# Performance work log

Measured on AMD Instinct MI355X. Metric: run time of the kernel, lower is better.

Reference implementation:

```python
import jax, jax.numpy as jnp
import numpy as np

LEAKY_SLOPE = 0.2  # alpha in the torch module
EPS = 1e-10

N_NODES = 100000
N_EDGES = 1600000
IN_F = 128
OUT_F = 64


def setup_inputs() -> dict:
    key = jax.random.key(0)
    k1, k2, k3, k4, k5 = jax.random.split(key, 5)
    h = jax.random.normal(k1, (N_NODES, IN_F), dtype=jnp.float32)
    W = jax.random.normal(k2, (IN_F, OUT_F), dtype=jnp.float32) * (1.0 / np.sqrt(IN_F))
    a1 = jax.random.normal(k3, (OUT_F,), dtype=jnp.float32) * 0.1
    a2 = jax.random.normal(k4, (OUT_F,), dtype=jnp.float32) * 0.1
    edge_index = jax.random.randint(k5, (2, N_EDGES), 0, N_NODES, dtype=jnp.int32)
    return {"h": h, "W": W, "a1": a1, "a2": a2, "edge_index": edge_index}


def reference(h, W, a1, a2, edge_index):
    # h: [N, in_f], W: [in_f, out_f], a1/a2: [out_f], edge_index: [2, E]
    N = h.shape[0]
    Wh = h @ W                                   # [N, out_f]
    row, col = edge_index[0], edge_index[1]      # [E]
    f1 = Wh @ a1                                 # [N]
    f2 = Wh @ a2                                 # [N]
    e = jax.nn.leaky_relu(f1[row] + f2[col], negative_slope=LEAKY_SLOPE)  # [E]
    e_exp = jnp.exp(e - jnp.max(e))              # global-max shift, as in torch code
    exp_sum = jax.ops.segment_sum(e_exp, row, num_segments=N)            # [N]
    alpha = e_exp / (exp_sum[row] + EPS)         # [E]  (dropout is identity in eval)
    weighted_Wh = Wh[col] * alpha[:, None]       # [E, out_f]
    h_prime = jax.ops.segment_sum(weighted_Wh, row, num_segments=N)      # [N, out_f]
    return jax.nn.elu(h_prime)                   # concat=True path
```

## Files before the change

### kernel.cpp

```cpp
#include <hip/hip_runtime.h>
#include <hip/hip_bf16.h>

#define N_NODES 100000
#define N_EDGES 1600000
#define IN_F 128
#define OUT_F 64

#define RPB 64
#define NB  1563
#define C_CHUNKS 250
#define CHUNK 6400
#define M_CNT (NB * C_CHUNKS)
#define SCANA_BLOCKS ((M_CNT + 1023) / 1024)

typedef __attribute__((ext_vector_type(8))) short short8;
typedef __attribute__((ext_vector_type(4))) float f32x4;

#define LDS_PITCH 136

__device__ __forceinline__ unsigned short f2bf(float x) {
    unsigned u = __float_as_uint(x);
    return (unsigned short)((u + 0x7FFFu + ((u >> 16) & 1u)) >> 16);
}
__device__ __forceinline__ float bf2f_u(unsigned short b) {
    return __uint_as_float((unsigned)b << 16);
}

__global__ __launch_bounds__(1024) void k_hist(
    const int* __restrict__ ei, int* __restrict__ cnt,
    const float* __restrict__ W, const float* __restrict__ a1,
    const float* __restrict__ a2, float* __restrict__ wa1, float* __restrict__ wa2)
{
    __shared__ int hl[NB];
    const int c = blockIdx.x;
    if (c == C_CHUNKS) {
        const int k = threadIdx.x;
        if (k < IN_F) {
            float s1 = 0.f, s2 = 0.f;
            #pragma unroll 8
            for (int f = 0; f < OUT_F; f++) {
                const float w = W[k * OUT_F + f];
                s1 += w * a1[f];
                s2 += w * a2[f];
            }
            wa1[k] = s1;
            wa2[k] = s2;
        }
        return;
    }
    for (int i = threadIdx.x; i < NB; i += 1024) hl[i] = 0;
    __syncthreads();
    const int e0 = c * CHUNK;
    for (int i = threadIdx.x; i < CHUNK; i += 1024)
        atomicAdd(&hl[ei[e0 + i] >> 6], 1);
    __syncthreads();
    for (int b = threadIdx.x; b < NB; b += 1024)
        cnt[b * C_CHUNKS + c] = hl[b];
}

__global__ __launch_bounds__(256) void k_gemm(
    const float* __restrict__ h, const float* __restrict__ W,
    const float* __restrict__ wa1, const float* __restrict__ wa2,
    unsigned short* __restrict__ Whb, float* __restrict__ f1, float* __restrict__ f2)
{
    __shared__ unsigned short Wt[OUT_F * LDS_PITCH];
    __shared__ unsigned short Al[16 * LDS_PITCH];

    const int tid  = threadIdx.x;
    const int lane = tid & 63;
    const int wav  = tid >> 6;
    const int quad = lane >> 4;
    const int nl   = lane & 15;

    for (int i = tid; i < IN_F * OUT_F; i += 256) {
        const int k = i >> 6, f = i & 63;
        Wt[f * LDS_PITCH + k] = f2bf(W[i]);
    }
    __syncthreads();

    short8 bfrag[4];
    #pragma unroll
    for (int ch = 0; ch < 4; ch++)
        bfrag[ch] = *(const short8*)&Wt[(wav * 16 + nl) * LDS_PITCH + ch * 32 + quad * 8];

    const int srow = tid >> 4;
    const int sc   = tid & 15;
    float w1r[8], w2r[8];
    #pragma unroll
    for (int j = 0; j < 8; j++) { w1r[j] = wa1[sc * 8 + j]; w2r[j] = wa2[sc * 8 + j]; }

    const int ntiles = N_NODES / 16;
    for (int tile = blockIdx.x; tile < ntiles; tile += gridDim.x) {
        const int base = tile * 16;
        __syncthreads();

        const float4 v0 = *(const float4*)&h[(base + srow) * IN_F + sc * 8];
        const float4 v1 = *(const float4*)&h[(base + srow) * IN_F + sc * 8 + 4];
        float p1 = v0.x * w1r[0] + v0.y * w1r[1] + v0.z * w1r[2] + v0.w * w1r[3]
                 + v1.x * w1r[4] + v1.y * w1r[5] + v1.z * w1r[6] + v1.w * w1r[7];
        float p2 = v0.x * w2r[0] + v0.y * w2r[1] + v0.z * w2r[2] + v0.w * w2r[3]
                 + v1.x * w2r[4] + v1.y * w2r[5] + v1.z * w2r[6] + v1.w * w2r[7];
        #pragma unroll
        for (int m = 8; m >= 1; m >>= 1) {
            p1 += __shfl_xor(p1, m, 64);
            p2 += __shfl_xor(p2, m, 64);
        }
        if (sc == 0) { f1[base + srow] = p1; f2[base + srow] = p2; }

        uint4 packed;
        packed.x = (unsigned)f2bf(v0.x) | ((unsigned)f2bf(v0.y) << 16);
        packed.y = (unsigned)f2bf(v0.z) | ((unsigned)f2bf(v0.w) << 16);
        packed.z = (unsigned)f2bf(v1.x) | ((unsigned)f2bf(v1.y) << 16);
        packed.w = (unsigned)f2bf(v1.z) | ((unsigned)f2bf(v1.w) << 16);
        *(uint4*)&Al[srow * LDS_PITCH + sc * 8] = packed;

        __syncthreads();

        f32x4 acc = {0.f, 0.f, 0.f, 0.f};
        #pragma unroll
        for (int ch = 0; ch < 4; ch++) {
            const short8 afrag = *(const short8*)&Al[nl * LDS_PITCH + ch * 32 + quad * 8];
            acc = __builtin_amdgcn_mfma_f32_16x16x32_bf16(afrag, bfrag[ch], acc, 0, 0, 0);
        }

        const int col = wav * 16 + nl;
        #pragma unroll
        for (int r = 0; r < 4; r++)
            Whb[(base + quad * 4 + r) * OUT_F + col] = f2bf(acc[r]);
    }
}

__global__ __launch_bounds__(256) void k_scanA(const int* __restrict__ cnt,
                                               int* __restrict__ bsum)
{
    __shared__ int sd[256];
    const int t = threadIdx.x;
    const int i0 = blockIdx.x * 1024 + t * 4;
    int s = 0;
    #pragma unroll
    for (int k = 0; k < 4; k++) {
        const int i = i0 + k;
        s += (i < M_CNT) ? cnt[i] : 0;
    }
    sd[t] = s; __syncthreads();
    for (int off = 128; off >= 1; off >>= 1) {
        if (t < off) sd[t] += sd[t + off];
        __syncthreads();
    }
    if (t == 0) bsum[blockIdx.x] = sd[0];
}

__global__ __launch_bounds__(256) void k_scanC(int* __restrict__ cnt,
                                               const int* __restrict__ bsum)
{
    __shared__ int red[256];
    __shared__ int ts[256];
    const int t = threadIdx.x;

    int pv = 0;
    for (int i = t; i < (int)blockIdx.x; i += 256) pv += bsum[i];
    red[t] = pv; __syncthreads();
    for (int off = 128; off >= 1; off >>= 1) {
        if (t < off) red[t] += red[t + off];
        __syncthreads();
    }
    const int bpref = red[0];

    const int i0 = blockIdx.x * 1024 + t * 4;
    int v[4]; int s = 0;
    #pragma unroll
    for (int k = 0; k < 4; k++) {
        const int i = i0 + k;
        v[k] = (i < M_CNT) ? cnt[i] : 0;
        s += v[k];
    }
    ts[t] = s; __syncthreads();
    for (int off = 1; off < 256; off <<= 1) {
        const int x = (t >= off) ? ts[t - off] : 0;
        __syncthreads();
        ts[t] += x;
        __syncthreads();
    }
    int excl = ts[t] - s + bpref;
    #pragma unroll
    for (int k = 0; k < 4; k++) {
        const int i = i0 + k;
        if (i < M_CNT) cnt[i] = excl;
        excl += v[k];
    }
}

__global__ __launch_bounds__(1024) void k_scatter(
    const int* __restrict__ ei,
    const float* __restrict__ f1,
    const float* __restrict__ f2,
    const int* __restrict__ cnt,
    uint2* __restrict__ pairs)
{
    __shared__ int cur[NB];
    const int c = blockIdx.x;
    for (int b = threadIdx.x; b < NB; b += 1024)
        cur[b] = cnt[b * C_CHUNKS + c];
    __syncthreads();

    const int e0 = c * CHUNK;
    for (int i = threadIdx.x; i < CHUNK; i += 1024) {
        const int r  = ei[e0 + i];
        const int cl = ei[N_EDGES + e0 + i];
        float x = f1[r] + f2[cl];
        x = (x >= 0.f) ? x : 0.2f * x;
        const float ee = __expf(x);
        const int pos = atomicAdd(&cur[r >> 6], 1);
        pairs[pos] = make_uint2(((unsigned)(r & 63) << 17) | (unsigned)cl,
                                __float_as_uint(ee));
    }
}

__global__ __launch_bounds__(256) void k_sort(
    const int* __restrict__ cnt,
    const uint2* __restrict__ pairs,
    uint2* __restrict__ pairs2,
    int* __restrict__ rowptr)
{
    __shared__ int cnt64[64];
    __shared__ int cur64[64];

    const int b   = blockIdx.x;
    const int tid = threadIdx.x;
    const int start = cnt[b * C_CHUNKS];
    const int end   = (b == NB - 1) ? N_EDGES : cnt[(b + 1) * C_CHUNKS];

    if (tid < 64) cnt64[tid] = 0;
    __syncthreads();

    for (int i = start + tid; i < end; i += 256)
        atomicAdd(&cnt64[pairs[i].x >> 17], 1);
    __syncthreads();

    if (tid < 64) {
        const int v = cnt64[tid];
        int s = v;
        #pragma unroll
        for (int off = 1; off < 64; off <<= 1) {
            const int x = __shfl_up(s, off, 64);
            if (tid >= off) s += x;
        }
        cur64[tid] = s - v;
        const int g = b * 64 + tid;
        if (g < N_NODES) rowptr[g] = start + s - v;
    }
    __syncthreads();

    for (int i = start + tid; i < end; i += 256) {
        const uint2 p = pairs[i];
        const int pos = atomicAdd(&cur64[p.x >> 17], 1);
        pairs2[start + pos] = p;
    }
    if (b == 0 && tid == 0) rowptr[N_NODES] = N_EDGES;
}

__global__ __launch_bounds__(256) void k_agg(
    const int* __restrict__ rowptr,
    const uint2* __restrict__ pairs2,
    const unsigned short* __restrict__ Whb,
    float* __restrict__ out)
{
    const int wid  = (blockIdx.x * 256 + threadIdx.x) >> 6;
    const int lane = threadIdx.x & 63;
    if (wid >= N_NODES) return;

    const int start = rowptr[wid];
    const int end   = rowptr[wid + 1];

    float acc = 0.f, s = 0.f;
    int j = start;

    for (; j + 8 <= end; j += 8) {
        uint2 p[8];
        #pragma unroll
        for (int k = 0; k < 8; k++) p[k] = pairs2[j + k];
        float wh[8];
        #pragma unroll
        for (int k = 0; k < 8; k++)
            wh[k] = bf2f_u(Whb[(((int)(p[k].x & 0x1FFFFu)) << 6) + lane]);
        #pragma unroll
        for (int k = 0; k < 8; k++) {
            const float ee = __uint_as_float(p[k].y);
            acc += ee * wh[k];
            s   += ee;
        }
    }
    for (; j + 4 <= end; j += 4) {
        uint2 p[4];
        #pragma unroll
        for (int k = 0; k < 4; k++) p[k] = pairs2[j + k];
        float wh[4];
        #pragma unroll
        for (int k = 0; k < 4; k++)
            wh[k] = bf2f_u(Whb[(((int)(p[k].x & 0x1FFFFu)) << 6) + lane]);
        #pragma unroll
        for (int k = 0; k < 4; k++) {
            const float ee = __uint_as_float(p[k].y);
            acc += ee * wh[k];
            s   += ee;
        }
    }
    for (; j < end; j++) {
        const uint2 p = pairs2[j];
        const float ee = __uint_as_float(p.y);
        acc += ee * bf2f_u(Whb[(((int)(p.x & 0x1FFFFu)) << 6) + lane]);
        s   += ee;
    }

    const float r = acc / (s + 1e-10f);
    out[wid * OUT_F + lane] = (r > 0.f) ? r : expm1f(r);
}

extern "C" void kernel_launch(void* const* d_in, const int* in_sizes, int n_in,
                              void* d_out, int out_size, void* d_ws, size_t ws_size,
                              hipStream_t stream) {
    const float* h  = (const float*)d_in[0];
    const float* W  = (const float*)d_in[1];
    const float* a1 = (const float*)d_in[2];
    const float* a2 = (const float*)d_in[3];
    const int* ei   = (const int*)d_in[4];
    float* out      = (float*)d_out;

    float* ws = (float*)d_ws;
    unsigned short* Whb = (unsigned short*)ws;
    float* f1     = ws + 3200000;
    float* f2     = f1 + N_NODES;
    float* wa1    = f2 + N_NODES;
    float* wa2    = wa1 + 128;
    int*   cnt    = (int*)(wa2 + 128);
    int*   bsum   = cnt + M_CNT;
    int*   rowptr = bsum + 384;
    int*   pad    = rowptr + 100002;
    if ((size_t)(pad - (int*)ws) & 1) pad++;
    uint2* pairs  = (uint2*)pad;
    uint2* pairs2 = pairs + N_EDGES;

    k_hist   <<<C_CHUNKS + 1, 1024, 0, stream>>>(ei, cnt, W, a1, a2, wa1, wa2);
    k_scanA  <<<SCANA_BLOCKS, 256, 0, stream>>>(cnt, bsum);
    k_scanC  <<<SCANA_BLOCKS, 256, 0, stream>>>(cnt, bsum);
    k_gemm   <<<1250, 256, 0, stream>>>(h, W, wa1, wa2, Whb, f1, f2);
    k_scatter<<<C_CHUNKS, 1024, 0, stream>>>(ei, f1, f2, cnt, pairs);
    k_sort   <<<NB, 256, 0, stream>>>(cnt, pairs, pairs2, rowptr);
    k_agg    <<<(N_NODES * 64 + 255) / 256, 256, 0, stream>>>(rowptr, pairs2, Whb, out);
}
```

Before: 228.3 us.

## Fuse per-bucket sort and aggregation into one block-level LDS-atomic kernel

Removes the second-level sort kernel and the per-row aggregation kernel. Each block now takes its 64-row bucket of unsorted pairs, splits it across four waves, and accumulates weighted Wh rows and exp sums into shared memory with atomics before applying normalization and ELU. This saves a full pass that reads and writes the pairs array, plus one launch. In exchange it adds LDS atomic contention and uses fewer, larger blocks.

Result: slower. 774.6 us (+239.3%).

```diff
diff --git a/kernel.cpp b/kernel.cpp
--- a/kernel.cpp
+++ b/kernel.cpp
@@ -216,69 +216,35 @@
     }
 }
 
-__global__ __launch_bounds__(256) void k_sort(
+__global__ __launch_bounds__(256) void k_aggb(
     const int* __restrict__ cnt,
     const uint2* __restrict__ pairs,
-    uint2* __restrict__ pairs2,
-    int* __restrict__ rowptr)
-{
-    __shared__ int cnt64[64];
-    __shared__ int cur64[64];
-
-    const int b   = blockIdx.x;
-    const int tid = threadIdx.x;
+    const unsigned short* __restrict__ Whb,
+    float* __restrict__ out)
+{
+    __shared__ float acc[64 * 64];
+    __shared__ float ssum[64];
+
+    const int b    = blockIdx.x;
+    const int tid  = threadIdx.x;
+    const int lane = tid & 63;
+    const int wav  = tid >> 6;
+
+    for (int i = tid; i < 64 * 64; i += 256) acc[i] = 0.f;
+    if (tid < 64) ssum[tid] = 0.f;
+    __syncthreads();
+
     const int start = cnt[b * C_CHUNKS];
     const int end   = (b == NB - 1) ? N_EDGES : cnt[(b + 1) * C_CHUNKS];
-
-    if (tid < 64) cnt64[tid] = 0;
-    __syncthreads();
-
-    for (int i = start + tid; i < end; i += 256)
-        atomicAdd(&cnt64[pairs[i].x >> 17], 1);
-    __syncthreads();
-
-    if (tid < 64) {
-        const int v = cnt64[tid];
-        int s = v;
-        #pragma unroll
-        for (int off = 1; off < 64; off <<= 1) {
-            const int x = __shfl_up(s, off, 64);
-            if (tid >= off) s += x;
-        }
-        cur64[tid] = s - v;
-        const int g = b * 64 + tid;
-        if (g < N_NODES) rowptr[g] = start + s - v;
-    }
-    __syncthreads();
-
-    for (int i = start + tid; i < end; i += 256) {
-        const uint2 p = pairs[i];
-        const int pos = atomicAdd(&cur64[p.x >> 17], 1);
-        pairs2[start + pos] = p;
-    }
-    if (b == 0 && tid == 0) rowptr[N_NODES] = N_EDGES;
-}
-
-__global__ __launch_bounds__(256) void k_agg(
-    const int* __restrict__ rowptr,
-    const uint2* __restrict__ pairs2,
-    const unsigned short* __restrict__ Whb,
-    float* __restrict__ out)
-{
-    const int wid  = (blockIdx.x * 256 + threadIdx.x) >> 6;
-    const int lane = threadIdx.x & 63;
-    if (wid >= N_NODES) return;
-
-    const int start = rowptr[wid];
-    const int end   = rowptr[wid + 1];
-
-    float acc = 0.f, s = 0.f;
-    int j = start;
-
-    for (; j + 8 <= end; j += 8) {
+    const int len   = end - start;
+    const int w0 = start + (len * wav) / 4;
+    const int w1 = start + (len * (wav + 1)) / 4;
+
+    int j = w0;
+    for (; j + 8 <= w1; j += 8) {
         uint2 p[8];
         #pragma unroll
-        for (int k = 0; k < 8; k++) p[k] = pairs2[j + k];
+        for (int k = 0; k < 8; k++) p[k] = pairs[j + k];
         float wh[8];
         #pragma unroll
         for (int k = 0; k < 8; k++)
@@ -286,14 +252,15 @@
         #pragma unroll
         for (int k = 0; k < 8; k++) {
             const float ee = __uint_as_float(p[k].y);
-            acc += ee * wh[k];
-            s   += ee;
-        }
-    }
-    for (; j + 4 <= end; j += 4) {
+            const int rl   = (int)(p[k].x >> 17);
+            atomicAdd(&acc[rl * 64 + lane], ee * wh[k]);
+            if (lane == 0) atomicAdd(&ssum[rl], ee);
+        }
+    }
+    for (; j + 4 <= w1; j += 4) {
         uint2 p[4];
         #pragma unroll
-        for (int k = 0; k < 4; k++) p[k] = pairs2[j + k];
+        for (int k = 0; k < 4; k++) p[k] = pairs[j + k];
         float wh[4];
         #pragma unroll
         for (int k = 0; k < 4; k++)
@@ -301,19 +268,28 @@
         #pragma unroll
         for (int k = 0; k < 4; k++) {
             const float ee = __uint_as_float(p[k].y);
-            acc += ee * wh[k];
-            s   += ee;
-        }
-    }
-    for (; j < end; j++) {
-        const uint2 p = pairs2[j];
+            const int rl   = (int)(p[k].x >> 17);
+            atomicAdd(&acc[rl * 64 + lane], ee * wh[k]);
+            if (lane == 0) atomicAdd(&ssum[rl], ee);
+        }
+    }
+    for (; j < w1; j++) {
+        const uint2 p = pairs[j];
         const float ee = __uint_as_float(p.y);
-        acc += ee * bf2f_u(Whb[(((int)(p.x & 0x1FFFFu)) << 6) + lane]);
-        s   += ee;
-    }
-
-    const float r = acc / (s + 1e-10f);
-    out[wid * OUT_F + lane] = (r > 0.f) ? r : expm1f(r);
+        const int rl   = (int)(p.x >> 17);
+        atomicAdd(&acc[rl * 64 + lane],
+                  ee * bf2f_u(Whb[(((int)(p.x & 0x1FFFFu)) << 6) + lane]));
+        if (lane == 0) atomicAdd(&ssum[rl], ee);
+    }
+    __syncthreads();
+
+    for (int rl = wav; rl < 64; rl += 4) {
+        const int g = b * 64 + rl;
+        if (g < N_NODES) {
+            const float r = acc[rl * 64 + lane] / (ssum[rl] + 1e-10f);
+            out[g * OUT_F + lane] = (r > 0.f) ? r : expm1f(r);
+        }
+    }
 }
 
 extern "C" void kernel_launch(void* const* d_in, const int* in_sizes, int n_in,
@@ -338,13 +314,11 @@
     int*   pad    = rowptr + 100002;
     if ((size_t)(pad - (int*)ws) & 1) pad++;
     uint2* pairs  = (uint2*)pad;
-    uint2* pairs2 = pairs + N_EDGES;
 
     k_hist   <<<C_CHUNKS + 1, 1024, 0, stream>>>(ei, cnt, W, a1, a2, wa1, wa2);
     k_scanA  <<<SCANA_BLOCKS, 256, 0, stream>>>(cnt, bsum);
     k_scanC  <<<SCANA_BLOCKS, 256, 0, stream>>>(cnt, bsum);
     k_gemm   <<<1250, 256, 0, stream>>>(h, W, wa1, wa2, Whb, f1, f2);
     k_scatter<<<C_CHUNKS, 1024, 0, stream>>>(ei, f1, f2, cnt, pairs);
-    k_sort   <<<NB, 256, 0, stream>>>(cnt, pairs, pairs2, rowptr);
-    k_agg    <<<(N_NODES * 64 + 255) / 256, 256, 0, stream>>>(rowptr, pairs2, Whb, out);
-}
+    k_aggb   <<<NB, 256, 0, stream>>>(cnt, pairs, Whb, out);
+}
```

## Fuse histogram with GEMM and bucket sort with aggregation kernels

Applied to the files above, without the earlier changes.

Merges the edge histogram and the node GEMM into one launch, with blocks split by role and LDS shared through a union. Each GEMM block now computes W·a1/W·a2 itself, so the separate reduction block goes away. Also fuses the per-bucket sort with aggregation: each block sorts its 64-row bucket, keeps the row pointers in LDS, then its 4 waves each aggregate 16 rows, with no global rowptr and no separate agg launch. This cuts the launch count from 7 to 5 and the rowptr round trip, but lowers aggregation parallelism to 4 waves per 64 rows and repeats the wa computation in every GEMM block.

After: 281.8 us. +23.4%, slower.

```diff
diff --git a/kernel.cpp b/kernel.cpp
--- a/kernel.cpp
+++ b/kernel.cpp
@@ -12,6 +12,7 @@
 #define CHUNK 6400
 #define M_CNT (NB * C_CHUNKS)
 #define SCANA_BLOCKS ((M_CNT + 1023) / 1024)
+#define GEMM_BLOCKS 1250
 
 typedef __attribute__((ext_vector_type(8))) short short8;
 typedef __attribute__((ext_vector_type(4))) float f32x4;
@@ -26,47 +27,35 @@
     return __uint_as_float((unsigned)b << 16);
 }
 
-__global__ __launch_bounds__(1024) void k_hist(
+__global__ __launch_bounds__(256) void k_histgemm(
     const int* __restrict__ ei, int* __restrict__ cnt,
-    const float* __restrict__ W, const float* __restrict__ a1,
-    const float* __restrict__ a2, float* __restrict__ wa1, float* __restrict__ wa2)
-{
-    __shared__ int hl[NB];
-    const int c = blockIdx.x;
-    if (c == C_CHUNKS) {
-        const int k = threadIdx.x;
-        if (k < IN_F) {
-            float s1 = 0.f, s2 = 0.f;
-            #pragma unroll 8
-            for (int f = 0; f < OUT_F; f++) {
-                const float w = W[k * OUT_F + f];
-                s1 += w * a1[f];
-                s2 += w * a2[f];
-            }
-            wa1[k] = s1;
-            wa2[k] = s2;
-        }
+    const float* __restrict__ h, const float* __restrict__ W,
+    const float* __restrict__ a1, const float* __restrict__ a2,
+    unsigned short* __restrict__ Whb, float* __restrict__ f1, float* __restrict__ f2)
+{
+    __shared__ __align__(16) union {
+        int hl[NB];
+        struct {
+            unsigned short Wt[OUT_F * LDS_PITCH];
+            unsigned short Al[16 * LDS_PITCH];
+        } g;
+    } u;
+
+    const int bid = blockIdx.x;
+    const int tid = threadIdx.x;
+
+    if (bid < C_CHUNKS) {
+        for (int i = tid; i < NB; i += 256) u.hl[i] = 0;
+        __syncthreads();
+        const int e0 = bid * CHUNK;
+        for (int i = tid; i < CHUNK; i += 256)
+            atomicAdd(&u.hl[ei[e0 + i] >> 6], 1);
+        __syncthreads();
+        for (int b = tid; b < NB; b += 256)
+            cnt[b * C_CHUNKS + bid] = u.hl[b];
         return;
     }
-    for (int i = threadIdx.x; i < NB; i += 1024) hl[i] = 0;
-    __syncthreads();
-    const int e0 = c * CHUNK;
-    for (int i = threadIdx.x; i < CHUNK; i += 1024)
-        atomicAdd(&hl[ei[e0 + i] >> 6], 1);
-    __syncthreads();
-    for (int b = threadIdx.x; b < NB; b += 1024)
-        cnt[b * C_CHUNKS + c] = hl[b];
-}
-
-__global__ __launch_bounds__(256) void k_gemm(
-    const float* __restrict__ h, const float* __restrict__ W,
-    const float* __restrict__ wa1, const float* __restrict__ wa2,
-    unsigned short* __restrict__ Whb, float* __restrict__ f1, float* __restrict__ f2)
-{
-    __shared__ unsigned short Wt[OUT_F * LDS_PITCH];
-    __shared__ unsigned short Al[16 * LDS_PITCH];
-
-    const int tid  = threadIdx.x;
+
     const int lane = tid & 63;
     const int wav  = tid >> 6;
     const int quad = lane >> 4;
@@ -74,23 +63,33 @@
 
     for (int i = tid; i < IN_F * OUT_F; i += 256) {
         const int k = i >> 6, f = i & 63;
-        Wt[f * LDS_PITCH + k] = f2bf(W[i]);
-    }
-    __syncthreads();
-
-    short8 bfrag[4];
-    #pragma unroll
-    for (int ch = 0; ch < 4; ch++)
-        bfrag[ch] = *(const short8*)&Wt[(wav * 16 + nl) * LDS_PITCH + ch * 32 + quad * 8];
+        u.g.Wt[f * LDS_PITCH + k] = f2bf(W[i]);
+    }
 
     const int srow = tid >> 4;
     const int sc   = tid & 15;
     float w1r[8], w2r[8];
     #pragma unroll
-    for (int j = 0; j < 8; j++) { w1r[j] = wa1[sc * 8 + j]; w2r[j] = wa2[sc * 8 + j]; }
+    for (int j = 0; j < 8; j++) {
+        float s1 = 0.f, s2 = 0.f;
+        const float* wr = &W[(sc * 8 + j) * OUT_F];
+        #pragma unroll 8
+        for (int f = 0; f < OUT_F; f++) {
+            const float w = wr[f];
+            s1 += w * a1[f];
+            s2 += w * a2[f];
+        }
+        w1r[j] = s1; w2r[j] = s2;
+    }
+    __syncthreads();
+
+    short8 bfrag[4];
+    #pragma unroll
+    for (int ch = 0; ch < 4; ch++)
+        bfrag[ch] = *(const short8*)&u.g.Wt[(wav * 16 + nl) * LDS_PITCH + ch * 32 + quad * 8];
 
     const int ntiles = N_NODES / 16;
-    for (int tile = blockIdx.x; tile < ntiles; tile += gridDim.x) {
+    for (int tile = bid - C_CHUNKS; tile < ntiles; tile += GEMM_BLOCKS) {
         const int base = tile * 16;
         __syncthreads();
 
@@ -112,14 +111,14 @@
         packed.y = (unsigned)f2bf(v0.z) | ((unsigned)f2bf(v0.w) << 16);
         packed.z = (unsigned)f2bf(v1.x) | ((unsigned)f2bf(v1.y) << 16);
         packed.w = (unsigned)f2bf(v1.z) | ((unsigned)f2bf(v1.w) << 16);
-        *(uint4*)&Al[srow * LDS_PITCH + sc * 8] = packed;
+        *(uint4*)&u.g.Al[srow * LDS_PITCH + sc * 8] = packed;
 
         __syncthreads();
 
         f32x4 acc = {0.f, 0.f, 0.f, 0.f};
         #pragma unroll
         for (int ch = 0; ch < 4; ch++) {
-            const short8 afrag = *(const short8*)&Al[nl * LDS_PITCH + ch * 32 + quad * 8];
+            const short8 afrag = *(const short8*)&u.g.Al[nl * LDS_PITCH + ch * 32 + quad * 8];
             acc = __builtin_amdgcn_mfma_f32_16x16x32_bf16(afrag, bfrag[ch], acc, 0, 0, 0);
         }
 
@@ -216,25 +215,31 @@
     }
 }
 
-__global__ __launch_bounds__(256) void k_sort(
+__global__ __launch_bounds__(256) void k_sortagg(
     const int* __restrict__ cnt,
     const uint2* __restrict__ pairs,
     uint2* __restrict__ pairs2,
-    int* __restrict__ rowptr)
+    const unsigned short* __restrict__ Whb,
+    float* __restrict__ out)
 {
     __shared__ int cnt64[64];
     __shared__ int cur64[64];
-
-    const int b   = blockIdx.x;
-    const int tid = threadIdx.x;
+    __shared__ int rp[65];
+
+    const int b    = blockIdx.x;
+    const int tid  = threadIdx.x;
+    const int lane = tid & 63;
+    const int wav  = tid >> 6;
+
     const int start = cnt[b * C_CHUNKS];
     const int end   = (b == NB - 1) ? N_EDGES : cnt[(b + 1) * C_CHUNKS];
+    const int len   = end - start;
 
     if (tid < 64) cnt64[tid] = 0;
     __syncthreads();
 
-    for (int i = start + tid; i < end; i += 256)
-        atomicAdd(&cnt64[pairs[i].x >> 17], 1);
+    for (int i = tid; i < len; i += 256)
+        atomicAdd(&cnt64[pairs[start + i].x >> 17], 1);
     __syncthreads();
 
     if (tid < 64) {
@@ -245,75 +250,68 @@
             const int x = __shfl_up(s, off, 64);
             if (tid >= off) s += x;
         }
+        rp[tid]    = s - v;
         cur64[tid] = s - v;
-        const int g = b * 64 + tid;
-        if (g < N_NODES) rowptr[g] = start + s - v;
-    }
-    __syncthreads();
-
-    for (int i = start + tid; i < end; i += 256) {
-        const uint2 p = pairs[i];
+        if (tid == 63) rp[64] = s;
+    }
+    __syncthreads();
+
+    for (int i = tid; i < len; i += 256) {
+        const uint2 p = pairs[start + i];
         const int pos = atomicAdd(&cur64[p.x >> 17], 1);
         pairs2[start + pos] = p;
     }
-    if (b == 0 && tid == 0) rowptr[N_NODES] = N_EDGES;
-}
-
-__global__ __launch_bounds__(256) void k_agg(
-    const int* __restrict__ rowptr,
-    const uint2* __restrict__ pairs2,
-    const unsigned short* __restrict__ Whb,
-    float* __restrict__ out)
-{
-    const int wid  = (blockIdx.x * 256 + threadIdx.x) >> 6;
-    const int lane = threadIdx.x & 63;
-    if (wid >= N_NODES) return;
-
-    const int start = rowptr[wid];
-    const int end   = rowptr[wid + 1];
-
-    float acc = 0.f, s = 0.f;
-    int j = start;
-
-    for (; j + 8 <= end; j += 8) {
-        uint2 p[8];
-        #pragma unroll
-        for (int k = 0; k < 8; k++) p[k] = pairs2[j + k];
-        float wh[8];
-        #pragma unroll
-        for (int k = 0; k < 8; k++)
-            wh[k] = bf2f_u(Whb[(((int)(p[k].x & 0x1FFFFu)) << 6) + lane]);
-        #pragma unroll
-        for (int k = 0; k < 8; k++) {
-            const float ee = __uint_as_float(p[k].y);
-            acc += ee * wh[k];
+    __syncthreads();
+
+    const uint2* __restrict__ pb = pairs2 + start;
+    for (int t = 0; t < 16; t++) {
+        const int n = wav * 16 + t;
+        const int g = b * 64 + n;
+        if (g >= N_NODES) break;
+        const int j1 = rp[n + 1];
+        int j = rp[n];
+        float acc = 0.f, s = 0.f;
+
+        for (; j + 8 <= j1; j += 8) {
+            uint2 p[8];
+            #pragma unroll
+            for (int k = 0; k < 8; k++) p[k] = pb[j + k];
+            float wh[8];
+            #pragma unroll
+            for (int k = 0; k < 8; k++)
+                wh[k] = bf2f_u(Whb[(((int)(p[k].x & 0x1FFFFu)) << 6) + lane]);
+            #pragma unroll
+            for (int k = 0; k < 8; k++) {
+                const float ee = __uint_as_float(p[k].y);
+                acc += ee * wh[k];
+                s   += ee;
+            }
+        }
+        for (; j + 4 <= j1; j += 4) {
+            uint2 p[4];
+            #pragma unroll
+            for (int k = 0; k < 4; k++) p[k] = pb[j + k];
+            float wh[4];
+            #pragma unroll
+            for (int k = 0; k < 4; k++)
+                wh[k] = bf2f_u(Whb[(((int)(p[k].x & 0x1FFFFu)) << 6) + lane]);
+            #pragma unroll
+            for (int k = 0; k < 4; k++) {
+                const float ee = __uint_as_float(p[k].y);
+                acc += ee * wh[k];
+                s   += ee;
+            }
+        }
+        for (; j < j1; j++) {
+            const uint2 p = pb[j];
+            const float ee = __uint_as_float(p.y);
+            acc += ee * bf2f_u(Whb[(((int)(p.x & 0x1FFFFu)) << 6) + lane]);
             s   += ee;
         }
-    }
-    for (; j + 4 <= end; j += 4) {
-        uint2 p[4];
-        #pragma unroll
-        for (int k = 0; k < 4; k++) p[k] = pairs2[j + k];
-        float wh[4];
-        #pragma unroll
-        for (int k = 0; k < 4; k++)
-            wh[k] = bf2f_u(Whb[(((int)(p[k].x & 0x1FFFFu)) << 6) + lane]);
-        #pragma unroll
-        for (int k = 0; k < 4; k++) {
-            const float ee = __uint_as_float(p[k].y);
-            acc += ee * wh[k];
-            s   += ee;
-        }
-    }
-    for (; j < end; j++) {
-        const uint2 p = pairs2[j];
-        const float ee = __uint_as_float(p.y);
-        acc += ee * bf2f_u(Whb[(((int)(p.x & 0x1FFFFu)) << 6) + lane]);
-        s   += ee;
-    }
-
-    const float r = acc / (s + 1e-10f);
-    out[wid * OUT_F + lane] = (r > 0.f) ? r : expm1f(r);
+
+        const float r = acc / (s + 1e-10f);
+        out[g * OUT_F + lane] = (r > 0.f) ? r : expm1f(r);
+    }
 }
 
 extern "C" void kernel_launch(void* const* d_in, const int* in_sizes, int n_in,
@@ -340,11 +338,10 @@
     uint2* pairs  = (uint2*)pad;
     uint2* pairs2 = pairs + N_EDGES;
 
-    k_hist   <<<C_CHUNKS + 1, 1024, 0, stream>>>(ei, cnt, W, a1, a2, wa1, wa2);
-    k_scanA  <<<SCANA_BLOCKS, 256, 0, stream>>>(cnt, bsum);
-    k_scanC  <<<SCANA_BLOCKS, 256, 0, stream>>>(cnt, bsum);
-    k_gemm   <<<1250, 256, 0, stream>>>(h, W, wa1, wa2, Whb, f1, f2);
-    k_scatter<<<C_CHUNKS, 1024, 0, stream>>>(ei, f1, f2, cnt, pairs);
-    k_sort   <<<NB, 256, 0, stream>>>(cnt, pairs, pairs2, rowptr);
-    k_agg    <<<(N_NODES * 64 + 255) / 256, 256, 0, stream>>>(rowptr, pairs2, Whb, out);
-}
+    k_histgemm<<<C_CHUNKS + GEMM_BLOCKS, 256, 0, stream>>>(ei, cnt, h, W, a1, a2,
+                                                           Whb, f1, f2);
+    k_scanA   <<<SCANA_BLOCKS, 256, 0, stream>>>(cnt, bsum);
+    k_scanC   <<<SCANA_BLOCKS, 256, 0, stream>>>(cnt, bsum);
+    k_scatter <<<C_CHUNKS, 1024, 0, stream>>>(ei, f1, f2, cnt, pairs);
+    k_sortagg <<<NB, 256, 0, stream>>>(cnt, pairs, pairs2, Whb, out);
+}
```

## Build CSR with global atomic degree count and direct placement instead of bucket sort

Applied to the files above, without the earlier changes.

Replaces the two-level bucket sort (per-chunk histograms over 64-row buckets, scatter, then a per-bucket local sort) with a direct CSR build. A global atomic degree count runs over all edges, a scan over the 100k node degrees produces row pointers and cursors, and each edge then claims its final slot with a global atomicAdd. This drops the large chunk-by-bucket count matrix and scan, the intermediate pairs buffer and the whole k_sort pass. In exchange it relies on heavy global atomic traffic to random addresses, and the order of edges within a row becomes nondeterministic.

Result: slower. 322.8 us (+41.4%).

```diff
diff --git a/kernel.cpp b/kernel.cpp
--- a/kernel.cpp
+++ b/kernel.cpp
@@ -6,12 +6,10 @@
 #define IN_F 128
 #define OUT_F 64
 
-#define RPB 64
-#define NB  1563
-#define C_CHUNKS 250
-#define CHUNK 6400
-#define M_CNT (NB * C_CHUNKS)
-#define SCANA_BLOCKS ((M_CNT + 1023) / 1024)
+#define ZERO_BLOCKS 99
+#define CNT_BLOCKS 391
+#define SCAN_BLOCKS 98
+#define GEMM_BLOCKS 1250
 
 typedef __attribute__((ext_vector_type(8))) short short8;
 typedef __attribute__((ext_vector_type(4))) float f32x4;
@@ -26,14 +24,13 @@
     return __uint_as_float((unsigned)b << 16);
 }
 
-__global__ __launch_bounds__(1024) void k_hist(
-    const int* __restrict__ ei, int* __restrict__ cnt,
-    const float* __restrict__ W, const float* __restrict__ a1,
-    const float* __restrict__ a2, float* __restrict__ wa1, float* __restrict__ wa2)
-{
-    __shared__ int hl[NB];
-    const int c = blockIdx.x;
-    if (c == C_CHUNKS) {
+__global__ __launch_bounds__(1024) void k_zero(
+    int* __restrict__ deg, const float* __restrict__ W,
+    const float* __restrict__ a1, const float* __restrict__ a2,
+    float* __restrict__ wa1, float* __restrict__ wa2)
+{
+    const int bid = blockIdx.x;
+    if (bid == SCAN_BLOCKS) {
         const int k = threadIdx.x;
         if (k < IN_F) {
             float s1 = 0.f, s2 = 0.f;
@@ -48,14 +45,82 @@
         }
         return;
     }
-    for (int i = threadIdx.x; i < NB; i += 1024) hl[i] = 0;
-    __syncthreads();
-    const int e0 = c * CHUNK;
-    for (int i = threadIdx.x; i < CHUNK; i += 1024)
-        atomicAdd(&hl[ei[e0 + i] >> 6], 1);
-    __syncthreads();
-    for (int b = threadIdx.x; b < NB; b += 1024)
-        cnt[b * C_CHUNKS + c] = hl[b];
+    const int i = bid * 1024 + threadIdx.x;
+    if (i < N_NODES) deg[i] = 0;
+}
+
+__global__ __launch_bounds__(1024) void k_count(
+    const int* __restrict__ ei, int* __restrict__ deg)
+{
+    const int base = blockIdx.x * 4096 + threadIdx.x;
+    #pragma unroll
+    for (int k = 0; k < 4; k++) {
+        const int e = base + k * 1024;
+        if (e < N_EDGES) atomicAdd(&deg[ei[e]], 1);
+    }
+}
+
+__global__ __launch_bounds__(256) void k_scanA(const int* __restrict__ deg,
+                                               int* __restrict__ bsum)
+{
+    __shared__ int sd[256];
+    const int t = threadIdx.x;
+    const int i0 = blockIdx.x * 1024 + t * 4;
+    int s = 0;
+    #pragma unroll
+    for (int k = 0; k < 4; k++) {
+        const int i = i0 + k;
+        s += (i < N_NODES) ? deg[i] : 0;
+    }
+    sd[t] = s; __syncthreads();
+    for (int off = 128; off >= 1; off >>= 1) {
+        if (t < off) sd[t] += sd[t + off];
+        __syncthreads();
+    }
+    if (t == 0) bsum[blockIdx.x] = sd[0];
+}
+
+__global__ __launch_bounds__(256) void k_scanC(const int* __restrict__ deg,
+                                               const int* __restrict__ bsum,
+                                               int* __restrict__ rowptr,
+                                               int* __restrict__ cur)
+{
+    __shared__ int red[256];
+    __shared__ int ts[256];
+    const int t = threadIdx.x;
+
+    int pv = 0;
+    for (int i = t; i < (int)blockIdx.x; i += 256) pv += bsum[i];
+    red[t] = pv; __syncthreads();
+    for (int off = 128; off >= 1; off >>= 1) {
+        if (t < off) red[t] += red[t + off];
+        __syncthreads();
+    }
+    const int bpref = red[0];
+
+    const int i0 = blockIdx.x * 1024 + t * 4;
+    int v[4]; int s = 0;
+    #pragma unroll
+    for (int k = 0; k < 4; k++) {
+        const int i = i0 + k;
+        v[k] = (i < N_NODES) ? deg[i] : 0;
+        s += v[k];
+    }
+    ts[t] = s; __syncthreads();
+    for (int off = 1; off < 256; off <<= 1) {
+        const int x = (t >= off) ? ts[t - off] : 0;
+        __syncthreads();
+        ts[t] += x;
+        __syncthreads();
+    }
+    int excl = ts[t] - s + bpref;
+    #pragma unroll
+    for (int k = 0; k < 4; k++) {
+        const int i = i0 + k;
+        if (i < N_NODES) { rowptr[i] = excl; cur[i] = excl; }
+        excl += v[k];
+    }
+    if (blockIdx.x == 0 && t == 0) rowptr[N_NODES] = N_EDGES;
 }
 
 __global__ __launch_bounds__(256) void k_gemm(
@@ -130,133 +195,38 @@
     }
 }
 
-__global__ __launch_bounds__(256) void k_scanA(const int* __restrict__ cnt,
-                                               int* __restrict__ bsum)
-{
-    __shared__ int sd[256];
-    const int t = threadIdx.x;
-    const int i0 = blockIdx.x * 1024 + t * 4;
-    int s = 0;
-    #pragma unroll
-    for (int k = 0; k < 4; k++) {
-        const int i = i0 + k;
-        s += (i < M_CNT) ? cnt[i] : 0;
-    }
-    sd[t] = s; __syncthreads();
-    for (int off = 128; off >= 1; off >>= 1) {
-        if (t < off) sd[t] += sd[t + off];
-        __syncthreads();
-    }
-    if (t == 0) bsum[blockIdx.x] = sd[0];
-}
-
-__global__ __launch_bounds__(256) void k_scanC(int* __restrict__ cnt,
-                                               const int* __restrict__ bsum)
-{
-    __shared__ int red[256];
-    __shared__ int ts[256];
-    const int t = threadIdx.x;
-
-    int pv = 0;
-    for (int i = t; i < (int)blockIdx.x; i += 256) pv += bsum[i];
-    red[t] = pv; __syncthreads();
-    for (int off = 128; off >= 1; off >>= 1) {
-        if (t < off) red[t] += red[t + off];
-        __syncthreads();
-    }
-    const int bpref = red[0];
-
-    const int i0 = blockIdx.x * 1024 + t * 4;
-    int v[4]; int s = 0;
-    #pragma unroll
-    for (int k = 0; k < 4; k++) {
-        const int i = i0 + k;
-        v[k] = (i < M_CNT) ? cnt[i] : 0;
-        s += v[k];
-    }
-    ts[t] = s; __syncthreads();
-    for (int off = 1; off < 256; off <<= 1) {
-        const int x = (t >= off) ? ts[t - off] : 0;
-        __syncthreads();
-        ts[t] += x;
-        __syncthreads();
-    }
-    int excl = ts[t] - s + bpref;
-    #pragma unroll
-    for (int k = 0; k < 4; k++) {
-        const int i = i0 + k;
-        if (i < M_CNT) cnt[i] = excl;
-        excl += v[k];
-    }
-}
-
-__global__ __launch_bounds__(1024) void k_scatter(
+__global__ __launch_bounds__(1024) void k_place(
     const int* __restrict__ ei,
     const float* __restrict__ f1,
     const float* __restrict__ f2,
-    const int* __restrict__ cnt,
-    uint2* __restrict__ pairs)
-{
-    __shared__ int cur[NB];
-    const int c = blockIdx.x;
-    for (int b = threadIdx.x; b < NB; b += 1024)
-        cur[b] = cnt[b * C_CHUNKS + c];
-    __syncthreads();
-
-    const int e0 = c * CHUNK;
-    for (int i = threadIdx.x; i < CHUNK; i += 1024) {
-        const int r  = ei[e0 + i];
-        const int cl = ei[N_EDGES + e0 + i];
-        float x = f1[r] + f2[cl];
+    int* __restrict__ cur,
+    uint2* __restrict__ pairs2)
+{
+    const int base = blockIdx.x * 4096 + threadIdx.x;
+
+    int r[4], cl[4];
+    bool ok[4];
+    #pragma unroll
+    for (int k = 0; k < 4; k++) {
+        const int e = base + k * 1024;
+        ok[k] = (e < N_EDGES);
+        r[k]  = ok[k] ? ei[e] : 0;
+        cl[k] = ok[k] ? ei[N_EDGES + e] : 0;
+    }
+    float ee[4];
+    #pragma unroll
+    for (int k = 0; k < 4; k++) {
+        float x = f1[r[k]] + f2[cl[k]];
         x = (x >= 0.f) ? x : 0.2f * x;
-        const float ee = __expf(x);
-        const int pos = atomicAdd(&cur[r >> 6], 1);
-        pairs[pos] = make_uint2(((unsigned)(r & 63) << 17) | (unsigned)cl,
-                                __float_as_uint(ee));
-    }
-}
-
-__global__ __launch_bounds__(256) void k_sort(
-    const int* __restrict__ cnt,
-    const uint2* __restrict__ pairs,
-    uint2* __restrict__ pairs2,
-    int* __restrict__ rowptr)
-{
-    __shared__ int cnt64[64];
-    __shared__ int cur64[64];
-
-    const int b   = blockIdx.x;
-    const int tid = threadIdx.x;
-    const int start = cnt[b * C_CHUNKS];
-    const int end   = (b == NB - 1) ? N_EDGES : cnt[(b + 1) * C_CHUNKS];
-
-    if (tid < 64) cnt64[tid] = 0;
-    __syncthreads();
-
-    for (int i = start + tid; i < end; i += 256)
-        atomicAdd(&cnt64[pairs[i].x >> 17], 1);
-    __syncthreads();
-
-    if (tid < 64) {
-        const int v = cnt64[tid];
-        int s = v;
-        #pragma unroll
-        for (int off = 1; off < 64; off <<= 1) {
-            const int x = __shfl_up(s, off, 64);
-            if (tid >= off) s += x;
-        }
-        cur64[tid] = s - v;
-        const int g = b * 64 + tid;
-        if (g < N_NODES) rowptr[g] = start + s - v;
-    }
-    __syncthreads();
-
-    for (int i = start + tid; i < end; i += 256) {
-        const uint2 p = pairs[i];
-        const int pos = atomicAdd(&cur64[p.x >> 17], 1);
-        pairs2[start + pos] = p;
-    }
-    if (b == 0 && tid == 0) rowptr[N_NODES] = N_EDGES;
+        ee[k] = __expf(x);
+    }
+    #pragma unroll
+    for (int k = 0; k < 4; k++) {
+        if (ok[k]) {
+            const int pos = atomicAdd(&cur[r[k]], 1);
+            pairs2[pos] = make_uint2((unsigned)cl[k], __float_as_uint(ee[k]));
+        }
+    }
 }
 
 __global__ __launch_bounds__(256) void k_agg(
@@ -332,19 +302,19 @@
     float* f2     = f1 + N_NODES;
     float* wa1    = f2 + N_NODES;
     float* wa2    = wa1 + 128;
-    int*   cnt    = (int*)(wa2 + 128);
-    int*   bsum   = cnt + M_CNT;
-    int*   rowptr = bsum + 384;
-    int*   pad    = rowptr + 100002;
+    int*   deg    = (int*)(wa2 + 128);
+    int*   bsum   = deg + N_NODES;
+    int*   rowptr = bsum + 128;
+    int*   cur    = rowptr + 100001;
+    int*   pad    = cur + N_NODES;
     if ((size_t)(pad - (int*)ws) & 1) pad++;
-    uint2* pairs  = (uint2*)pad;
-    uint2* pairs2 = pairs + N_EDGES;
-
-    k_hist   <<<C_CHUNKS + 1, 1024, 0, stream>>>(ei, cnt, W, a1, a2, wa1, wa2);
-    k_scanA  <<<SCANA_BLOCKS, 256, 0, stream>>>(cnt, bsum);
-    k_scanC  <<<SCANA_BLOCKS, 256, 0, stream>>>(cnt, bsum);
-    k_gemm   <<<1250, 256, 0, stream>>>(h, W, wa1, wa2, Whb, f1, f2);
-    k_scatter<<<C_CHUNKS, 1024, 0, stream>>>(ei, f1, f2, cnt, pairs);
-    k_sort   <<<NB, 256, 0, stream>>>(cnt, pairs, pairs2, rowptr);
-    k_agg    <<<(N_NODES * 64 + 255) / 256, 256, 0, stream>>>(rowptr, pairs2, Whb, out);
-}
+    uint2* pairs2 = (uint2*)pad;
+
+    k_zero  <<<ZERO_BLOCKS, 1024, 0, stream>>>(deg, W, a1, a2, wa1, wa2);
+    k_count <<<CNT_BLOCKS, 1024, 0, stream>>>(ei, deg);
+    k_scanA <<<SCAN_BLOCKS, 256, 0, stream>>>(deg, bsum);
+    k_scanC <<<SCAN_BLOCKS, 256, 0, stream>>>(deg, bsum, rowptr, cur);
+    k_gemm  <<<GEMM_BLOCKS, 256, 0, stream>>>(h, W, wa1, wa2, Whb, f1, f2);
+    k_place <<<CNT_BLOCKS, 1024, 0, stream>>>(ei, f1, f2, cur, pairs2);
+    k_agg   <<<(N_NODES * 64 + 255) / 256, 256, 0, stream>>>(rowptr, pairs2, Whb, out);
+}
```
